# Performance work log

Hardware: AMD Instinct MI355X
Metric: run time of the kernel (lower is better)

## Reference

```python
import jax, jax.numpy as jnp
import numpy as np

NEG_SLOPE = 0.2
MASK_FILL = -9e10


def setup_inputs() -> dict:
    key = jax.random.key(0)
    ks = jax.random.split(key, 8)
    B, N, D = 8, 2048, 64
    return {
        "opes_mask_adj": jax.random.randint(ks[0], (B, N, N), 0, 2, dtype=jnp.int32),
        "opes_mask_job": jax.random.randint(ks[1], (B, N, N), 0, 2, dtype=jnp.int32),
        "batch_idxes": jnp.arange(B, dtype=jnp.int64),
        "feats": jax.random.normal(ks[2], (B, N, D), dtype=jnp.float32),
        "W_ope": jax.random.normal(ks[3], (D, D), dtype=jnp.float32) * (1.0 / np.sqrt(D)),
        "attn_src": jax.random.normal(ks[4], (D,), dtype=jnp.float32) * (1.0 / np.sqrt(D)),
        "attn_dst": jax.random.normal(ks[5], (D,), dtype=jnp.float32) * (1.0 / np.sqrt(D)),
        "lambda_params": jax.random.normal(ks[6], (D, 2), dtype=jnp.float32),
    }


def reference(opes_mask_adj, opes_mask_job, batch_idxes, feats, W_ope, attn_src, attn_dst, lambda_params):
    # h_ope: [B, N, D]  (Linear with weight [out,in]: x @ W^T)
    h_ope = jnp.einsum("bnd,od->bno", feats, W_ope)
    a_src = h_ope @ attn_src  # [B, N]
    a_dst = h_ope @ attn_dst  # [B, N]
    e = a_src[:, :, None] + a_dst[:, None, :]  # [B, N, N]
    e = jnp.where(e >= 0, e, NEG_SLOPE * e)  # leaky relu

    mask_adj = opes_mask_adj[batch_idxes] == 1
    alpha_adj = jax.nn.softmax(jnp.where(mask_adj, e, MASK_FILL), axis=-1)
    h_adj = jnp.einsum("bnm,bmd->bnd", alpha_adj, h_ope)

    mask_job = opes_mask_job[batch_idxes] == 1
    alpha_job = jax.nn.softmax(jnp.where(mask_job, e, MASK_FILL), axis=-1)
    h_job = jnp.einsum("bnm,bmd->bnd", alpha_job, h_ope)

    # in_dim == out_dim -> identity residual (res_fc is None)
    lambdas = jax.nn.softmax(lambda_params, axis=1)  # [D, 2]
    lambda_adj, lambda_job = lambdas[:, 0], lambdas[:, 1]
    return lambda_adj * h_adj + lambda_job * h_job + feats
```

## Files before the change

### kernel.cpp

```cpp
#include <hip/hip_runtime.h>
#include <hip/hip_bf16.h>

#define B_ 8
#define N_ 2048
#define D_ 64

typedef __attribute__((ext_vector_type(8))) short bf16x8;
typedef __attribute__((ext_vector_type(4))) float f32x4;

__device__ inline unsigned short f32_bf16_rne(float f) {
    unsigned u = __float_as_uint(f);
    u += 0x7fffu + ((u >> 16) & 1u);
    return (unsigned short)(u >> 16);
}

__global__ __launch_bounds__(256) void prep_kernel(
    const float* __restrict__ feats, const float* __restrict__ W,
    const float* __restrict__ attn_src, const float* __restrict__ attn_dst,
    unsigned short* __restrict__ hT, float* __restrict__ a_src,
    float* __restrict__ a_dst) {
    __shared__ float w_lds[64 * 65];
    __shared__ float f_lds[32 * 64];
    __shared__ unsigned short hT_lds[64 * 40];

    const int t = threadIdx.x;
    const int b = blockIdx.x >> 6;
    const int rowbase = (blockIdx.x & 63) * 32;

#pragma unroll
    for (int k = 0; k < 4; k++) {
        int lin = (k * 256 + t) * 4;
        float4 v = *(const float4*)(W + lin);
        int o = lin >> 6, d = lin & 63;
        float* p = &w_lds[o * 65 + d];
        p[0] = v.x; p[1] = v.y; p[2] = v.z; p[3] = v.w;
    }
#pragma unroll
    for (int k = 0; k < 2; k++) {
        int lin = (k * 256 + t) * 4;
        float4 v = *(const float4*)(feats + (size_t)(b * N_ + rowbase) * D_ + lin);
        float* p = &f_lds[lin];
        p[0] = v.x; p[1] = v.y; p[2] = v.z; p[3] = v.w;
    }
    __syncthreads();

    const int w = t >> 6;
    const int o = t & 63;
    float acc[8] = {0.f, 0.f, 0.f, 0.f, 0.f, 0.f, 0.f, 0.f};
#pragma unroll 8
    for (int d = 0; d < 64; d++) {
        float wv = w_lds[o * 65 + d];
#pragma unroll
        for (int rr = 0; rr < 8; rr++)
            acc[rr] = fmaf(f_lds[(w * 8 + rr) * 64 + d], wv, acc[rr]);
    }
    float as_ = attn_src[o], ad_ = attn_dst[o];
#pragma unroll
    for (int rr = 0; rr < 8; rr++) {
        int row = rowbase + w * 8 + rr;
        float s1 = acc[rr] * as_;
        float s2 = acc[rr] * ad_;
#pragma unroll
        for (int off = 32; off; off >>= 1) {
            s1 += __shfl_xor(s1, off);
            s2 += __shfl_xor(s2, off);
        }
        if (o == 0) {
            a_src[b * N_ + row] = s1;
            a_dst[b * N_ + row] = s2;
        }
        hT_lds[o * 40 + w * 8 + rr] = f32_bf16_rne(acc[rr]);
    }
    __syncthreads();
    const int d = t >> 2, seg = t & 3;
    uint4 vv = *(const uint4*)(&hT_lds[d * 40 + seg * 8]);
    *(uint4*)(hT + ((size_t)(b * 64 + d) * N_ + rowbase + seg * 8)) = vv;
}

__global__ __launch_bounds__(256) void attn_kernel(
    const int* __restrict__ mask_adj, const int* __restrict__ mask_job,
    const int* __restrict__ batch_idxes,
    const unsigned short* __restrict__ hT, const float* __restrict__ a_src,
    const float* __restrict__ a_dst, const float* __restrict__ feats,
    const float* __restrict__ lambda_params, float* __restrict__ out) {
    __shared__ unsigned short hstage[64 * 128];

    const int t = threadIdx.x;
    const int b = blockIdx.x >> 5;
    const int ibase = (blockIdx.x & 31) * 64;
    const int wid = t >> 6, lane = t & 63;
    const int m = lane & 15, q = lane >> 4;
    const int irow0 = ibase + wid * 16;
    const int i_a = irow0 + m;

    int bi = batch_idxes[b];
    bi = (bi < 0) ? 0 : ((bi >= B_) ? (B_ - 1) : bi);
    const int* mA = mask_adj + (size_t)bi * N_ * N_ + (size_t)i_a * N_;
    const int* mJ = mask_job + (size_t)bi * N_ * N_ + (size_t)i_a * N_;
    const float asrc = a_src[b * N_ + i_a];
    const float* adst = a_dst + b * N_;

    f32x4 accA[4], accJ[4];
#pragma unroll
    for (int dd = 0; dd < 4; dd++) {
        accA[dd] = (f32x4){0.f, 0.f, 0.f, 0.f};
        accJ[dd] = (f32x4){0.f, 0.f, 0.f, 0.f};
    }
    float zA = 0.f, zJ = 0.f;

    const int sd = t >> 2, sseg = t & 3;
    const unsigned short* hrow = hT + (size_t)(b * 64 + sd) * N_;

    for (int jt = 0; jt < N_ / 128; jt++) {
        const int j0 = jt * 128;
#pragma unroll
        for (int c = 0; c < 4; c++) {
            int jc = sseg * 4 + c;
            uint4 v = *(const uint4*)(hrow + j0 + jc * 8);
            *(uint4*)(hstage + (sd * 16 + (jc ^ (sd & 15))) * 8) = v;
        }
        __syncthreads();

#pragma unroll
        for (int kk = 0; kk < 4; kk++) {
            const int jl = j0 + kk * 32 + q * 8;
            int4 a0 = *(const int4*)(mA + jl);
            int4 a1 = *(const int4*)(mA + jl + 4);
            int4 b0 = *(const int4*)(mJ + jl);
            int4 b1 = *(const int4*)(mJ + jl + 4);
            float4 d0 = *(const float4*)(adst + jl);
            float4 d1 = *(const float4*)(adst + jl + 4);
            int ma[8] = {a0.x, a0.y, a0.z, a0.w, a1.x, a1.y, a1.z, a1.w};
            int mj[8] = {b0.x, b0.y, b0.z, b0.w, b1.x, b1.y, b1.z, b1.w};
            float dv[8] = {d0.x, d0.y, d0.z, d0.w, d1.x, d1.y, d1.z, d1.w};
            bf16x8 fa, fj;
#pragma unroll
            for (int tt = 0; tt < 8; tt++) {
                float e = asrc + dv[tt];
                float le = fmaxf(e, 0.f) + 0.2f * fminf(e, 0.f);
                float p = __expf(le);
                float pa = (ma[tt] == 1) ? p : 0.f;
                float pj = (mj[tt] == 1) ? p : 0.f;
                zA += pa;
                zJ += pj;
                fa[tt] = (short)f32_bf16_rne(pa);
                fj[tt] = (short)f32_bf16_rne(pj);
            }
#pragma unroll
            for (int dd = 0; dd < 4; dd++) {
                int dn = dd * 16 + m;
                int jcl = kk * 4 + q;
                bf16x8 fb = *(const bf16x8*)(hstage +
                                (dn * 16 + (jcl ^ (dn & 15))) * 8);
                accA[dd] = __builtin_amdgcn_mfma_f32_16x16x32_bf16(fa, fb, accA[dd], 0, 0, 0);
                accJ[dd] = __builtin_amdgcn_mfma_f32_16x16x32_bf16(fj, fb, accJ[dd], 0, 0, 0);
            }
        }
        __syncthreads();
    }

    zA += __shfl_xor(zA, 16); zA += __shfl_xor(zA, 32);
    zJ += __shfl_xor(zJ, 16); zJ += __shfl_xor(zJ, 32);
    float* zbuf = (float*)hstage;
    if (q == 0) {
        zbuf[wid * 32 + m] = zA;
        zbuf[wid * 32 + 16 + m] = zJ;
    }
    __syncthreads();

    float invA[4], invJ[4];
#pragma unroll
    for (int r = 0; r < 4; r++) {
        invA[r] = 1.f / zbuf[wid * 32 + q * 4 + r];
        invJ[r] = 1.f / zbuf[wid * 32 + 16 + q * 4 + r];
    }
#pragma unroll
    for (int dd = 0; dd < 4; dd++) {
        int d = dd * 16 + m;
        float l0 = lambda_params[d * 2];
        float l1 = lambda_params[d * 2 + 1];
        float e0 = __expf(l0), e1 = __expf(l1);
        float inv = 1.f / (e0 + e1);
        float la = e0 * inv, lj = e1 * inv;
#pragma unroll
        for (int r = 0; r < 4; r++) {
            int i = irow0 + q * 4 + r;
            size_t off = (size_t)(b * N_ + i) * D_ + d;
            out[off] = la * accA[dd][r] * invA[r] + lj * accJ[dd][r] * invJ[r] + feats[off];
        }
    }
}

extern "C" void kernel_launch(void* const* d_in, const int* in_sizes, int n_in,
                              void* d_out, int out_size, void* d_ws, size_t ws_size,
                              hipStream_t stream) {
    const int* mask_adj = (const int*)d_in[0];
    const int* mask_job = (const int*)d_in[1];
    const int* batch_idxes = (const int*)d_in[2];
    const float* feats = (const float*)d_in[3];
    const float* W = (const float*)d_in[4];
    const float* attn_src = (const float*)d_in[5];
    const float* attn_dst = (const float*)d_in[6];
    const float* lambda_params = (const float*)d_in[7];
    float* out = (float*)d_out;

    unsigned short* hT = (unsigned short*)d_ws;
    float* a_src = (float*)((char*)d_ws + (size_t)B_ * 64 * N_ * 2);
    float* a_dst = a_src + B_ * N_;

    prep_kernel<<<B_ * (N_ / 32), 256, 0, stream>>>(feats, W, attn_src, attn_dst,
                                                    hT, a_src, a_dst);
    attn_kernel<<<B_ * (N_ / 64), 256, 0, stream>>>(mask_adj, mask_job, batch_idxes,
                                                    hT, a_src, a_dst, feats,
                                                    lambda_params, out);
}
```

Baseline: 307.2 us.

## Factor exp out of the attention loop, split keys across waves, drop LDS staging

Precomputes exp(a_dst) and exp(0.2*a_dst) per column so each score becomes a compare plus a multiply by per-row constants, with no per-element exp. Each block now covers 16 rows, and its four waves each take a quarter of the key range. Partial accumulators are reduced through LDS at the end. The h tiles are read straight from global memory instead of being staged in LDS. Row sums are computed with MFMA against a ones vector, and bf16 packing uses v_cvt_pk_bf16_f32. The exp factorisation can overflow for large scores, and there are now four times as many blocks, with an extra cross-wave reduction at the end.

```diff
diff --git a/kernel.cpp b/kernel.cpp
--- a/kernel.cpp
+++ b/kernel.cpp
@@ -1,5 +1,4 @@
 #include <hip/hip_runtime.h>
-#include <hip/hip_bf16.h>
 
 #define B_ 8
 #define N_ 2048
@@ -14,11 +13,17 @@
     return (unsigned short)(u >> 16);
 }
 
+__device__ inline unsigned cvt_pk_bf16(float lo, float hi) {
+    unsigned r;
+    asm("v_cvt_pk_bf16_f32 %0, %1, %2" : "=v"(r) : "v"(lo), "v"(hi));
+    return r;
+}
+
 __global__ __launch_bounds__(256) void prep_kernel(
     const float* __restrict__ feats, const float* __restrict__ W,
     const float* __restrict__ attn_src, const float* __restrict__ attn_dst,
     unsigned short* __restrict__ hT, float* __restrict__ a_src,
-    float* __restrict__ a_dst) {
+    float* __restrict__ F1, float* __restrict__ F2) {
     __shared__ float w_lds[64 * 65];
     __shared__ float f_lds[32 * 64];
     __shared__ unsigned short hT_lds[64 * 40];
@@ -67,7 +72,8 @@
         }
         if (o == 0) {
             a_src[b * N_ + row] = s1;
-            a_dst[b * N_ + row] = s2;
+            F1[b * N_ + row] = __expf(s2);
+            F2[b * N_ + row] = __expf(0.2f * s2);
         }
         hT_lds[o * 40 + w * 8 + rr] = f32_bf16_rne(acc[rr]);
     }
@@ -77,50 +83,45 @@
     *(uint4*)(hT + ((size_t)(b * 64 + d) * N_ + rowbase + seg * 8)) = vv;
 }
 
-__global__ __launch_bounds__(256) void attn_kernel(
+__global__ __launch_bounds__(256, 4) void attn_kernel(
     const int* __restrict__ mask_adj, const int* __restrict__ mask_job,
     const int* __restrict__ batch_idxes,
     const unsigned short* __restrict__ hT, const float* __restrict__ a_src,
-    const float* __restrict__ a_dst, const float* __restrict__ feats,
-    const float* __restrict__ lambda_params, float* __restrict__ out) {
-    __shared__ unsigned short hstage[64 * 128];
+    const float* __restrict__ F1, const float* __restrict__ F2,
+    const float* __restrict__ feats, const float* __restrict__ lambda_params,
+    float* __restrict__ out) {
+    __shared__ f32x4 redbuf[3][10][64];
 
     const int t = threadIdx.x;
-    const int b = blockIdx.x >> 5;
-    const int ibase = (blockIdx.x & 31) * 64;
+    const int b = blockIdx.x >> 7;
+    const int rowbase = (blockIdx.x & 127) * 16;
     const int wid = t >> 6, lane = t & 63;
     const int m = lane & 15, q = lane >> 4;
-    const int irow0 = ibase + wid * 16;
-    const int i_a = irow0 + m;
+    const int i_a = rowbase + m;
 
     int bi = batch_idxes[b];
     bi = (bi < 0) ? 0 : ((bi >= B_) ? (B_ - 1) : bi);
     const int* mA = mask_adj + (size_t)bi * N_ * N_ + (size_t)i_a * N_;
     const int* mJ = mask_job + (size_t)bi * N_ * N_ + (size_t)i_a * N_;
-    const float asrc = a_src[b * N_ + i_a];
-    const float* adst = a_dst + b * N_;
-
-    f32x4 accA[4], accJ[4];
-#pragma unroll
-    for (int dd = 0; dd < 4; dd++) {
-        accA[dd] = (f32x4){0.f, 0.f, 0.f, 0.f};
-        accJ[dd] = (f32x4){0.f, 0.f, 0.f, 0.f};
-    }
-    float zA = 0.f, zJ = 0.f;
-
-    const int sd = t >> 2, sseg = t & 3;
-    const unsigned short* hrow = hT + (size_t)(b * 64 + sd) * N_;
-
-    for (int jt = 0; jt < N_ / 128; jt++) {
-        const int j0 = jt * 128;
-#pragma unroll
-        for (int c = 0; c < 4; c++) {
-            int jc = sseg * 4 + c;
-            uint4 v = *(const uint4*)(hrow + j0 + jc * 8);
-            *(uint4*)(hstage + (sd * 16 + (jc ^ (sd & 15))) * 8) = v;
-        }
-        __syncthreads();
-
+
+    const float s = a_src[b * N_ + i_a];
+    const float cmpT = __expf(-s);
+    const float cT = __expf(-0.8f * s);
+    const float* f1p = F1 + b * N_;
+    const float* f2p = F2 + b * N_;
+    const unsigned short* hTb = hT + (size_t)b * 64 * N_;
+
+    f32x4 accA[4], accJ[4], accZA, accZJ;
+    const f32x4 z4 = {0.f, 0.f, 0.f, 0.f};
+#pragma unroll
+    for (int dd = 0; dd < 4; dd++) { accA[dd] = z4; accJ[dd] = z4; }
+    accZA = z4; accZJ = z4;
+    bf16x8 ones;
+#pragma unroll
+    for (int i = 0; i < 8; i++) ones[i] = (short)0x3F80;
+
+    for (int jt = 0; jt < 4; jt++) {
+        const int j0 = wid * 512 + jt * 128;
 #pragma unroll
         for (int kk = 0; kk < 4; kk++) {
             const int jl = j0 + kk * 32 + q * 8;
@@ -128,65 +129,84 @@
             int4 a1 = *(const int4*)(mA + jl + 4);
             int4 b0 = *(const int4*)(mJ + jl);
             int4 b1 = *(const int4*)(mJ + jl + 4);
-            float4 d0 = *(const float4*)(adst + jl);
-            float4 d1 = *(const float4*)(adst + jl + 4);
+            float4 g0 = *(const float4*)(f1p + jl);
+            float4 g1 = *(const float4*)(f1p + jl + 4);
+            float4 h0 = *(const float4*)(f2p + jl);
+            float4 h1 = *(const float4*)(f2p + jl + 4);
             int ma[8] = {a0.x, a0.y, a0.z, a0.w, a1.x, a1.y, a1.z, a1.w};
             int mj[8] = {b0.x, b0.y, b0.z, b0.w, b1.x, b1.y, b1.z, b1.w};
-            float dv[8] = {d0.x, d0.y, d0.z, d0.w, d1.x, d1.y, d1.z, d1.w};
-            bf16x8 fa, fj;
-#pragma unroll
-            for (int tt = 0; tt < 8; tt++) {
-                float e = asrc + dv[tt];
-                float le = fmaxf(e, 0.f) + 0.2f * fminf(e, 0.f);
-                float p = __expf(le);
-                float pa = (ma[tt] == 1) ? p : 0.f;
-                float pj = (mj[tt] == 1) ? p : 0.f;
-                zA += pa;
-                zJ += pj;
-                fa[tt] = (short)f32_bf16_rne(pa);
-                fj[tt] = (short)f32_bf16_rne(pj);
-            }
+            float f1v[8] = {g0.x, g0.y, g0.z, g0.w, g1.x, g1.y, g1.z, g1.w};
+            float f2v[8] = {h0.x, h0.y, h0.z, h0.w, h1.x, h1.y, h1.z, h1.w};
+
+            unsigned ua[4], uj[4];
+#pragma unroll
+            for (int wp = 0; wp < 4; wp++) {
+                float p0 = (f1v[2 * wp] >= cmpT) ? f1v[2 * wp] : cT * f2v[2 * wp];
+                float p1 = (f1v[2 * wp + 1] >= cmpT) ? f1v[2 * wp + 1] : cT * f2v[2 * wp + 1];
+                float pa0 = (ma[2 * wp] == 1) ? p0 : 0.f;
+                float pa1 = (ma[2 * wp + 1] == 1) ? p1 : 0.f;
+                float pj0 = (mj[2 * wp] == 1) ? p0 : 0.f;
+                float pj1 = (mj[2 * wp + 1] == 1) ? p1 : 0.f;
+                ua[wp] = cvt_pk_bf16(pa0, pa1);
+                uj[wp] = cvt_pk_bf16(pj0, pj1);
+            }
+            union { uint4 u; bf16x8 v; } fa_, fj_;
+            fa_.u = make_uint4(ua[0], ua[1], ua[2], ua[3]);
+            fj_.u = make_uint4(uj[0], uj[1], uj[2], uj[3]);
+            bf16x8 fa = fa_.v, fj = fj_.v;
+
+            accZA = __builtin_amdgcn_mfma_f32_16x16x32_bf16(fa, ones, accZA, 0, 0, 0);
+            accZJ = __builtin_amdgcn_mfma_f32_16x16x32_bf16(fj, ones, accZJ, 0, 0, 0);
 #pragma unroll
             for (int dd = 0; dd < 4; dd++) {
-                int dn = dd * 16 + m;
-                int jcl = kk * 4 + q;
-                bf16x8 fb = *(const bf16x8*)(hstage +
-                                (dn * 16 + (jcl ^ (dn & 15))) * 8);
+                bf16x8 fb = *(const bf16x8*)(hTb + (size_t)(dd * 16 + m) * N_ + jl);
                 accA[dd] = __builtin_amdgcn_mfma_f32_16x16x32_bf16(fa, fb, accA[dd], 0, 0, 0);
                 accJ[dd] = __builtin_amdgcn_mfma_f32_16x16x32_bf16(fj, fb, accJ[dd], 0, 0, 0);
             }
         }
-        __syncthreads();
-    }
-
-    zA += __shfl_xor(zA, 16); zA += __shfl_xor(zA, 32);
-    zJ += __shfl_xor(zJ, 16); zJ += __shfl_xor(zJ, 32);
-    float* zbuf = (float*)hstage;
-    if (q == 0) {
-        zbuf[wid * 32 + m] = zA;
-        zbuf[wid * 32 + 16 + m] = zJ;
+    }
+
+    if (wid) {
+#pragma unroll
+        for (int c = 0; c < 4; c++) {
+            redbuf[wid - 1][c][lane] = accA[c];
+            redbuf[wid - 1][4 + c][lane] = accJ[c];
+        }
+        redbuf[wid - 1][8][lane] = accZA;
+        redbuf[wid - 1][9][lane] = accZJ;
     }
     __syncthreads();
-
-    float invA[4], invJ[4];
-#pragma unroll
-    for (int r = 0; r < 4; r++) {
-        invA[r] = 1.f / zbuf[wid * 32 + q * 4 + r];
-        invJ[r] = 1.f / zbuf[wid * 32 + 16 + q * 4 + r];
-    }
-#pragma unroll
-    for (int dd = 0; dd < 4; dd++) {
-        int d = dd * 16 + m;
-        float l0 = lambda_params[d * 2];
-        float l1 = lambda_params[d * 2 + 1];
-        float e0 = __expf(l0), e1 = __expf(l1);
-        float inv = 1.f / (e0 + e1);
-        float la = e0 * inv, lj = e1 * inv;
+    if (wid == 0) {
+#pragma unroll
+        for (int wv = 0; wv < 3; wv++) {
+#pragma unroll
+            for (int c = 0; c < 4; c++) {
+                accA[c] += redbuf[wv][c][lane];
+                accJ[c] += redbuf[wv][4 + c][lane];
+            }
+            accZA += redbuf[wv][8][lane];
+            accZJ += redbuf[wv][9][lane];
+        }
+        float invA[4], invJ[4];
 #pragma unroll
         for (int r = 0; r < 4; r++) {
-            int i = irow0 + q * 4 + r;
-            size_t off = (size_t)(b * N_ + i) * D_ + d;
-            out[off] = la * accA[dd][r] * invA[r] + lj * accJ[dd][r] * invJ[r] + feats[off];
+            invA[r] = 1.f / accZA[r];
+            invJ[r] = 1.f / accZJ[r];
+        }
+#pragma unroll
+        for (int dd = 0; dd < 4; dd++) {
+            int d = dd * 16 + m;
+            float l0 = lambda_params[d * 2];
+            float l1 = lambda_params[d * 2 + 1];
+            float e0 = __expf(l0), e1 = __expf(l1);
+            float inv = 1.f / (e0 + e1);
+            float la = e0 * inv, lj = e1 * inv;
+#pragma unroll
+            for (int r = 0; r < 4; r++) {
+                int i = rowbase + q * 4 + r;
+                size_t off = (size_t)(b * N_ + i) * D_ + d;
+                out[off] = la * accA[dd][r] * invA[r] + lj * accJ[dd][r] * invJ[r] + feats[off];
+            }
         }
     }
 }
@@ -206,11 +226,12 @@
 
     unsigned short* hT = (unsigned short*)d_ws;
     float* a_src = (float*)((char*)d_ws + (size_t)B_ * 64 * N_ * 2);
-    float* a_dst = a_src + B_ * N_;
+    float* F1 = a_src + B_ * N_;
+    float* F2 = F1 + B_ * N_;
 
     prep_kernel<<<B_ * (N_ / 32), 256, 0, stream>>>(feats, W, attn_src, attn_dst,
-                                                    hT, a_src, a_dst);
-    attn_kernel<<<B_ * (N_ / 64), 256, 0, stream>>>(mask_adj, mask_job, batch_idxes,
-                                                    hT, a_src, a_dst, feats,
+                                                    hT, a_src, F1, F2);
+    attn_kernel<<<B_ * (N_ / 16), 256, 0, stream>>>(mask_adj, mask_job, batch_idxes,
+                                                    hT, a_src, F1, F2, feats,
                                                     lambda_params, out);
 }
```

Measured after the change: 329.5 us. 7.3% more time.
